# Optimization experiments

Hardware: AMD Instinct MI355X
Metric: run time of the kernel (lower is better)

The kernel has to match this reference:

```python
import jax, jax.numpy as jnp
import numpy as np

SOFT_FACTOR = 1e-10


def setup_inputs() -> dict:
    key = jax.random.key(0)
    k1, k2 = jax.random.split(key)
    N, T, K, L = 32, 256, 8000, 64
    probs = jax.random.uniform(k1, (N, T, K), dtype=jnp.float32)
    targets = jax.random.randint(k2, (N, L), 0, K, dtype=jnp.int64)
    return {"probs": probs, "targets": targets}


def reference(probs, targets):
    # probs: [N, T, K], targets: [N, L] int labels in [0, K)
    N, T, K = probs.shape
    probs = probs + SOFT_FACTOR
    # Sum over time steps: [N, K]
    aggregation_probs = jnp.sum(probs, axis=1)
    # Batched histogram of targets over K classes: [N, K]
    rows = jnp.arange(N)[:, None]  # broadcast over L
    counted_targets = jnp.zeros((N, K), dtype=probs.dtype).at[rows, targets].add(1.0)
    mean_probs = aggregation_probs / T
    mean_targets = counted_targets / T
    loss = -jnp.sum(jnp.log(mean_probs) * mean_targets, axis=1)  # [N]
    return loss.mean()  # reduction='mean'
```

## Files before the change

kernel.cpp:

```cpp
#include <hip/hip_runtime.h>

constexpr int N_ = 32;
constexpr int T_ = 256;
constexpr int K_ = 8000;
constexpr int L_ = 64;

__global__ __launch_bounds__(256) void ACE_colsum_log(
    const float* __restrict__ probs,
    const int* __restrict__ targets,
    float* __restrict__ partial) {
    const int l = blockIdx.x;
    const int n = blockIdx.y;
    const int t = threadIdx.x;

    const int k = targets[n * L_ + l];
    const size_t idx = ((size_t)(n * T_ + t)) * (size_t)K_ + (size_t)k;
    float v = probs[idx];

    #pragma unroll
    for (int off = 32; off > 0; off >>= 1)
        v += __shfl_down(v, off, 64);

    __shared__ float wsum[4];
    const int wid = t >> 6;
    const int lane = t & 63;
    if (lane == 0) wsum[wid] = v;
    __syncthreads();

    if (t == 0) {
        const float s = wsum[0] + wsum[1] + wsum[2] + wsum[3];
        const float meanp = s * (1.0f / (float)T_) + 1e-10f;
        partial[n * L_ + l] = -logf(meanp);
    }
}

__global__ __launch_bounds__(256) void ACE_final_reduce(
    const float* __restrict__ partial,
    float* __restrict__ out) {
    const int tid = threadIdx.x;
    float s = 0.0f;
    #pragma unroll
    for (int i = tid; i < N_ * L_; i += 256)
        s += partial[i];

    #pragma unroll
    for (int off = 32; off > 0; off >>= 1)
        s += __shfl_down(s, off, 64);

    __shared__ float wsum[4];
    if ((tid & 63) == 0) wsum[tid >> 6] = s;
    __syncthreads();

    if (tid == 0) {
        const float total = wsum[0] + wsum[1] + wsum[2] + wsum[3];
        out[0] = total * (1.0f / ((float)N_ * (float)T_));
    }
}

extern "C" void kernel_launch(void* const* d_in, const int* in_sizes, int n_in,
                              void* d_out, int out_size, void* d_ws, size_t ws_size,
                              hipStream_t stream) {
    const float* probs = (const float*)d_in[0];
    const int* targets = (const int*)d_in[1];
    float* out = (float*)d_out;
    float* partial = (float*)d_ws;

    dim3 grid1(L_, N_);
    ACE_colsum_log<<<grid1, 256, 0, stream>>>(probs, targets, partial);
    ACE_final_reduce<<<1, 256, 0, stream>>>(partial, out);
}
```

Measured before the change: 18.17 us.

## Restructure gather so lanes map to targets and time is chunk-reduced

The gather kernel now assigns the 64 lanes of a wavefront to the 64 target labels and its 16 waves to 16 time steps. Each 1024-thread block covers one sample and one 16-step time chunk. Partial sums over the chunk are reduced through LDS and written per (n, chunk, l). The finishing kernel sums the 16 chunks, applies the log and averages. This cuts the block count from 2048 to 512, removes the per-block shuffle reductions, and loads each target once per wave instead of broadcasting it, at the cost of a heavier single-block final kernel.

```diff
diff --git a/kernel.cpp b/kernel.cpp
--- a/kernel.cpp
+++ b/kernel.cpp
@@ -4,57 +4,60 @@
 constexpr int T_ = 256;
 constexpr int K_ = 8000;
 constexpr int L_ = 64;
+constexpr int TCH = 16;
+constexpr int NBLK1 = N_ * (T_ / TCH);
 
-__global__ __launch_bounds__(256) void ACE_colsum_log(
+__global__ __launch_bounds__(1024) void ACE_gather(
     const float* __restrict__ probs,
     const int* __restrict__ targets,
-    float* __restrict__ partial) {
-    const int l = blockIdx.x;
-    const int n = blockIdx.y;
-    const int t = threadIdx.x;
+    float* __restrict__ ws2) {
+    const int w = threadIdx.x >> 6;
+    const int lane = threadIdx.x & 63;
+    const int n = blockIdx.x >> 4;
+    const int chunk = blockIdx.x & 15;
+    const int t = chunk * TCH + w;
 
-    const int k = targets[n * L_ + l];
-    const size_t idx = ((size_t)(n * T_ + t)) * (size_t)K_ + (size_t)k;
-    float v = probs[idx];
+    const int k = targets[(n << 6) + lane];
+    const float v = probs[((size_t)(n * T_ + t)) * (size_t)K_ + (size_t)k];
 
-    #pragma unroll
-    for (int off = 32; off > 0; off >>= 1)
-        v += __shfl_down(v, off, 64);
-
-    __shared__ float wsum[4];
-    const int wid = t >> 6;
-    const int lane = t & 63;
-    if (lane == 0) wsum[wid] = v;
+    __shared__ float lds[TCH * 64];
+    lds[(w << 6) + lane] = v;
     __syncthreads();
 
-    if (t == 0) {
-        const float s = wsum[0] + wsum[1] + wsum[2] + wsum[3];
-        const float meanp = s * (1.0f / (float)T_) + 1e-10f;
-        partial[n * L_ + l] = -logf(meanp);
+    if (w == 0) {
+        float s = 0.0f;
+        #pragma unroll
+        for (int j = 0; j < TCH; ++j)
+            s += lds[(j << 6) + lane];
+        ws2[(((n << 4) + chunk) << 6) + lane] = s;
     }
 }
 
-__global__ __launch_bounds__(256) void ACE_final_reduce(
-    const float* __restrict__ partial,
+__global__ __launch_bounds__(256) void ACE_finish(
+    const float* __restrict__ ws2,
     float* __restrict__ out) {
     const int tid = threadIdx.x;
     float s = 0.0f;
     #pragma unroll
-    for (int i = tid; i < N_ * L_; i += 256)
-        s += partial[i];
-
+    for (int j = 0; j < 8; ++j) {
+        const int c = tid + (j << 8);
+        const int n = c >> 6;
+        const int l = c & 63;
+        float cs = 0.0f;
+        #pragma unroll
+        for (int ch = 0; ch < 16; ++ch)
+            cs += ws2[(((n << 4) + ch) << 6) + l];
+        s += -logf(cs * (1.0f / (float)T_) + 1e-10f);
+    }
     #pragma unroll
     for (int off = 32; off > 0; off >>= 1)
         s += __shfl_down(s, off, 64);
-
     __shared__ float wsum[4];
     if ((tid & 63) == 0) wsum[tid >> 6] = s;
     __syncthreads();
-
-    if (tid == 0) {
-        const float total = wsum[0] + wsum[1] + wsum[2] + wsum[3];
-        out[0] = total * (1.0f / ((float)N_ * (float)T_));
-    }
+    if (tid == 0)
+        out[0] = (wsum[0] + wsum[1] + wsum[2] + wsum[3])
+                 * (1.0f / ((float)N_ * (float)T_));
 }
 
 extern "C" void kernel_launch(void* const* d_in, const int* in_sizes, int n_in,
@@ -63,9 +66,8 @@
     const float* probs = (const float*)d_in[0];
     const int* targets = (const int*)d_in[1];
     float* out = (float*)d_out;
-    float* partial = (float*)d_ws;
+    float* ws2 = (float*)d_ws;
 
-    dim3 grid1(L_, N_);
-    ACE_colsum_log<<<grid1, 256, 0, stream>>>(probs, targets, partial);
-    ACE_final_reduce<<<1, 256, 0, stream>>>(partial, out);
+    ACE_gather<<<NBLK1, 1024, 0, stream>>>(probs, targets, ws2);
+    ACE_finish<<<1, 256, 0, stream>>>(ws2, out);
 }
```

Result: no change. 17.96 us (-1.2%).
